# Optimization experiments

Hardware: AMD Instinct MI355X
Metric: run time of the kernel (lower is better)

## Reference

```python
import jax, jax.numpy as jnp
import numpy as np

B, LI, LJ, D = 32, 512, 512, 512
NN_DIM = 256  # agg output dim = 2*NN_DIM = 512


def setup_inputs() -> dict:
    key = jax.random.key(0)
    k1, k2, k3 = jax.random.split(key, 3)
    i = jax.random.normal(k1, (B, LI, D), dtype=jnp.float32)
    j = jax.random.normal(k2, (B, LJ, D), dtype=jnp.float32)
    W_agg = jax.random.normal(k3, (D, 2 * NN_DIM), dtype=jnp.float32) * (1.0 / np.sqrt(D))
    b_agg = jnp.zeros((2 * NN_DIM,), dtype=jnp.float32)
    return {"i": i, "j": j, "W_agg": W_agg, "b_agg": b_agg}


def _agg(x, W, b):
    # shared aggregation net: Dense(2*nn_dim) + tanh, then mean-pool over time
    # x: [B, L, D] -> [B, 2*nn_dim]
    return jnp.mean(jnp.tanh(jnp.einsum('bld,dh->blh', x, W) + b), axis=1)


def reference(i, j, W_agg, b_agg):
    # cross-attention scores: [B, Li, Lj]
    weight = jnp.einsum('bik,bjk->bij', i, j)
    # row softmax (over Lj) -> weights to aggregate j per i-position
    weight_j = jax.nn.softmax(weight, axis=2)
    # column softmax (over Li) -> weights to aggregate i per j-position
    weight_i = jax.nn.softmax(weight, axis=1)
    weighted_i = jnp.einsum('bij,bid->bjd', weight_i, i)  # [B, Lj, D]
    weighted_j = jnp.einsum('bij,bjd->bid', weight_j, j)  # [B, Li, D]
    output_i = jnp.abs(i - weighted_j)  # [B, Li, D]
    output_j = jnp.abs(j - weighted_i)  # [B, Lj, D]
    oi = _agg(output_i, W_agg, b_agg)   # [B, 2*nn_dim]
    oj = _agg(output_j, W_agg, b_agg)   # [B, 2*nn_dim]
    # K.mean(K.stack([oi, oj], axis=1), axis=1)
    return 0.5 * (oi + oj)
```

## Files before the change

kernel.cpp:

```cpp
#include <hip/hip_runtime.h>
#include <math.h>

#define B_ 32
#define L_ 512
#define D_ 512
#define H_ 512

typedef unsigned short u16;
typedef _Float16 h16;
typedef h16 half8 __attribute__((ext_vector_type(8)));
typedef float f32x4 __attribute__((ext_vector_type(4)));

#define SW(r, c) ((c) ^ (((r) >> 1) & 3))

typedef __attribute__((address_space(1))) void gvoid;
typedef __attribute__((address_space(3))) void svoid;
__device__ __forceinline__ void async_cp16(const void* g, void* l) {
    __builtin_amdgcn_global_load_lds((gvoid*)g, (svoid*)l, 16, 0, 0);
}

__device__ __forceinline__ u16 f2h(float x) {
    h16 h = (h16)x;
    u16 r;
    __builtin_memcpy(&r, &h, 2);
    return r;
}
__device__ __forceinline__ float h2f(u16 u) {
    h16 h;
    __builtin_memcpy(&h, &u, 2);
    return (float)h;
}
__device__ __forceinline__ float fast_tanh(float x) {
    return 1.0f - 2.0f / (__expf(2.0f * x) + 1.0f);
}

__device__ __forceinline__ void xcd_decode16(int n, int& z, int& tile) {
    int xcd = n & 7, w = n >> 3;
    z = xcd + 8 * (w >> 4);
    tile = w & 15;
}

__global__ __launch_bounds__(256) void cvt_all(const float* __restrict__ I,
                                               const float* __restrict__ Jm,
                                               const float* __restrict__ W,
                                               u16* __restrict__ Ih, u16* __restrict__ IhT,
                                               u16* __restrict__ Jh, u16* __restrict__ JhT,
                                               u16* __restrict__ WT,
                                               float* __restrict__ out) {
    const int z = blockIdx.z;
    const float* src;
    u16* h;
    u16* hT;
    size_t base;
    if (z < 32) {
        src = I; h = Ih; hT = IhT; base = (size_t)z * 512 * 512;
    } else if (z < 64) {
        src = Jm; h = Jh; hT = JhT; base = (size_t)(z - 32) * 512 * 512;
    } else {
        src = W; h = nullptr; hT = WT; base = 0;
        out[(blockIdx.y * 8 + blockIdx.x) * 256 + threadIdx.x] = 0.0f;
    }
    const int r0 = blockIdx.y * 64, c0 = blockIdx.x * 64;
    __shared__ u16 t[64][66];
    const int tid = threadIdx.x;
    const int tr = tid >> 4, tc4 = (tid & 15) * 4;
#pragma unroll
    for (int rep = 0; rep < 4; ++rep) {
        int r = rep * 16 + tr;
        f32x4 v = *(const f32x4*)(src + base + (size_t)(r0 + r) * 512 + c0 + tc4);
        unsigned h0 = f2h(v[0]), h1 = f2h(v[1]), h2 = f2h(v[2]), h3 = f2h(v[3]);
        if (h)
            *(uint2*)(h + base + (size_t)(r0 + r) * 512 + c0 + tc4) =
                make_uint2(h0 | (h1 << 16), h2 | (h3 << 16));
        t[r][tc4] = (u16)h0; t[r][tc4 + 1] = (u16)h1;
        t[r][tc4 + 2] = (u16)h2; t[r][tc4 + 3] = (u16)h3;
    }
    __syncthreads();
#pragma unroll
    for (int rep = 0; rep < 4; ++rep) {
        int r = rep * 16 + tr;
        unsigned a = t[tc4][r], b = t[tc4 + 1][r], c = t[tc4 + 2][r], d = t[tc4 + 3][r];
        *(uint2*)(hT + base + (size_t)(c0 + r) * 512 + r0 + tc4) =
            make_uint2(a | (b << 16), c | (d << 16));
    }
}

__global__ __launch_bounds__(256, 2) void score_mfma(const u16* __restrict__ Ih,
                                                     const u16* __restrict__ Jh,
                                                     u16* __restrict__ P_un,
                                                     u16* __restrict__ P_unT,
                                                     float* __restrict__ rtmax,
                                                     float* __restrict__ rtsum,
                                                     float* __restrict__ ctmax,
                                                     float* __restrict__ ctsum) {
    int b, tile;
    xcd_decode16(blockIdx.x, b, tile);
    const int i0 = (tile >> 2) * 128, j0 = (tile & 3) * 128;
    __shared__ u16 Ah[128 * 32], Bh[128 * 32];
    const int tid = threadIdx.x;
    const int wave = tid >> 6, lane = tid & 63;
    const int wm = (wave >> 1) * 64, wn = (wave & 1) * 64;
    const int lr = lane & 15, q = lane >> 4;
    const size_t boff = (size_t)b * L_ * D_;
    const u16* Ibh = Ih + boff;
    const u16* Jbh = Jh + boff;

    f32x4 acc[4][4] = {};

    for (int k0 = 0; k0 < D_; k0 += 32) {
#pragma unroll
        for (int h = 0; h < 2; ++h) {
            int g = wave * 2 + h;
            int r = g * 16 + (lane >> 2);
            int cg = SW(r, lane & 3);
            async_cp16(Ibh + (size_t)(i0 + r) * D_ + k0 + cg * 8, (char*)Ah + g * 1024);
            async_cp16(Jbh + (size_t)(j0 + r) * D_ + k0 + cg * 8, (char*)Bh + g * 1024);
        }
        __syncthreads();
        half8 af[4], bf[4];
#pragma unroll
        for (int mi = 0; mi < 4; ++mi) {
            int r = wm + mi * 16 + lr;
            af[mi] = *(const half8*)&Ah[r * 32 + SW(r, q) * 8];
        }
#pragma unroll
        for (int ni = 0; ni < 4; ++ni) {
            int r = wn + ni * 16 + lr;
            bf[ni] = *(const half8*)&Bh[r * 32 + SW(r, q) * 8];
        }
#pragma unroll
        for (int mi = 0; mi < 4; ++mi)
#pragma unroll
            for (int ni = 0; ni < 4; ++ni)
                acc[mi][ni] = __builtin_amdgcn_mfma_f32_16x16x32_f16(af[mi], bf[ni], acc[mi][ni], 0, 0, 0);
        __syncthreads();
    }

    float rm[4][4];
#pragma unroll
    for (int mi = 0; mi < 4; ++mi)
#pragma unroll
        for (int r4 = 0; r4 < 4; ++r4) {
            float t = fmaxf(fmaxf(acc[mi][0][r4], acc[mi][1][r4]),
                            fmaxf(acc[mi][2][r4], acc[mi][3][r4]));
#pragma unroll
            for (int off = 1; off < 16; off <<= 1) t = fmaxf(t, __shfl_xor(t, off));
            rm[mi][r4] = t;
        }
    float cm[4];
#pragma unroll
    for (int ni = 0; ni < 4; ++ni) {
        float u = -1e30f;
#pragma unroll
        for (int mi = 0; mi < 4; ++mi)
#pragma unroll
            for (int r4 = 0; r4 < 4; ++r4) u = fmaxf(u, acc[mi][ni][r4]);
        u = fmaxf(u, __shfl_xor(u, 16));
        u = fmaxf(u, __shfl_xor(u, 32));
        cm[ni] = u;
    }

    u16* Pu_b = P_un + (size_t)b * L_ * L_;
    u16* PuT_b = P_unT + (size_t)b * L_ * L_;
    float rs[4][4] = {};
    float cs[4] = {};
#pragma unroll
    for (int mi = 0; mi < 4; ++mi)
#pragma unroll
        for (int ni = 0; ni < 4; ++ni) {
            int i_base = i0 + wm + mi * 16 + q * 4;
            int j = j0 + wn + ni * 16 + lr;
            unsigned pc[4];
#pragma unroll
            for (int r4 = 0; r4 < 4; ++r4) {
                float er = __expf(acc[mi][ni][r4] - rm[mi][r4]);
                rs[mi][r4] += er;
                Pu_b[(size_t)(i_base + r4) * L_ + j] = f2h(er);
                float ec = __expf(acc[mi][ni][r4] - cm[ni]);
                cs[ni] += ec;
                pc[r4] = f2h(ec);
            }
            *(uint2*)&PuT_b[(size_t)j * L_ + i_base] =
                make_uint2(pc[0] | (pc[1] << 16), pc[2] | (pc[3] << 16));
        }

    const int gr = (j0 + wn) >> 6;
    const int gc = (i0 + wm) >> 6;
#pragma unroll
    for (int mi = 0; mi < 4; ++mi)
#pragma unroll
        for (int r4 = 0; r4 < 4; ++r4) {
            float s = rs[mi][r4];
#pragma unroll
            for (int off = 1; off < 16; off <<= 1) s += __shfl_xor(s, off);
            if (lr == 0) {
                int i = i0 + wm + mi * 16 + q * 4 + r4;
                rtmax[((size_t)b * L_ + i) * 8 + gr] = rm[mi][r4];
                rtsum[((size_t)b * L_ + i) * 8 + gr] = s;
            }
        }
#pragma unroll
    for (int ni = 0; ni < 4; ++ni) {
        float s = cs[ni];
        s += __shfl_xor(s, 16);
        s += __shfl_xor(s, 32);
        if (q == 0) {
            int j = j0 + wn + ni * 16 + lr;
            ctmax[((size_t)b * L_ + j) * 8 + gc] = cm[ni];
            ctsum[((size_t)b * L_ + j) * 8 + gc] = s;
        }
    }
}

__global__ __launch_bounds__(256, 2) void absdiff_scaled(const u16* __restrict__ P_un,
                                                         const u16* __restrict__ P_unT,
                                                         const float* __restrict__ rtmax,
                                                         const float* __restrict__ rtsum,
                                                         const float* __restrict__ ctmax,
                                                         const float* __restrict__ ctsum,
                                                         const u16* __restrict__ JhT,
                                                         const u16* __restrict__ IhT,
                                                         const u16* __restrict__ Ih,
                                                         const u16* __restrict__ Jh,
                                                         u16* __restrict__ Xall) {
    int zz, tile;
    xcd_decode16(blockIdx.x, zz, tile);
    const int side = zz >> 5, b = zz & 31;
    const int a0 = (tile >> 2) * 128, d0 = (tile & 3) * 128;
    const u16* Pb = (side ? P_unT : P_un) + (size_t)b * L_ * L_;
    const float* tmax = (side ? ctmax : rtmax) + (size_t)b * L_ * 8;
    const float* tsum = (side ? ctsum : rtsum) + (size_t)b * L_ * 8;
    const u16* Vt = (side ? IhT : JhT) + (size_t)b * D_ * L_;
    const u16* Oh = (side ? Jh : Ih) + (size_t)b * L_ * D_;
    u16* Xb = Xall + (size_t)zz * L_ * D_;

    __shared__ u16 As[128 * 32], Bs[128 * 32];
    __shared__ float sc[8][128];
    const int tid = threadIdx.x;
    const int wave = tid >> 6, lane = tid & 63;
    const int wm = (wave >> 1) * 64, wn = (wave & 1) * 64;
    const int lr = lane & 15, q = lane >> 4;

    if (tid < 128) {
        const float* tm = tmax + (size_t)(a0 + tid) * 8;
        const float* ts = tsum + (size_t)(a0 + tid) * 8;
        f32x4 m0 = *(const f32x4*)tm, m1 = *(const f32x4*)(tm + 4);
        f32x4 s0 = *(const f32x4*)ts, s1 = *(const f32x4*)(ts + 4);
        float m = fmaxf(fmaxf(fmaxf(m0[0], m0[1]), fmaxf(m0[2], m0[3])),
                        fmaxf(fmaxf(m1[0], m1[1]), fmaxf(m1[2], m1[3])));
        float e0 = __expf(m0[0] - m), e1 = __expf(m0[1] - m);
        float e2 = __expf(m0[2] - m), e3 = __expf(m0[3] - m);
        float e4 = __expf(m1[0] - m), e5 = __expf(m1[1] - m);
        float e6 = __expf(m1[2] - m), e7 = __expf(m1[3] - m);
        float inv = 1.0f / (e0 * s0[0] + e1 * s0[1] + e2 * s0[2] + e3 * s0[3] +
                            e4 * s1[0] + e5 * s1[1] + e6 * s1[2] + e7 * s1[3]);
        sc[0][tid] = e0 * inv; sc[1][tid] = e1 * inv;
        sc[2][tid] = e2 * inv; sc[3][tid] = e3 * inv;
        sc[4][tid] = e4 * inv; sc[5][tid] = e5 * inv;
        sc[6][tid] = e6 * inv; sc[7][tid] = e7 * inv;
    }
    __syncthreads();

    f32x4 acc[4][4] = {};

    for (int k0 = 0; k0 < L_; k0 += 32) {
#pragma unroll
        for (int h = 0; h < 2; ++h) {
            int g = wave * 2 + h;
            int r = g * 16 + (lane >> 2);
            int cg = SW(r, lane & 3);
            async_cp16(Pb + (size_t)(a0 + r) * L_ + k0 + cg * 8, (char*)As + g * 1024);
            async_cp16(Vt + (size_t)(d0 + r) * L_ + k0 + cg * 8, (char*)Bs + g * 1024);
        }
        __syncthreads();
        const int gk = k0 >> 6;
        half8 af[4], bf[4];
#pragma unroll
        for (int mi = 0; mi < 4; ++mi) {
            int r = wm + mi * 16 + lr;
            h16 s = (h16)sc[gk][r];
            half8 s8 = {s, s, s, s, s, s, s, s};
            af[mi] = *(const half8*)&As[r * 32 + SW(r, q) * 8] * s8;
        }
#pragma unroll
        for (int ni = 0; ni < 4; ++ni) {
            int r = wn + ni * 16 + lr;
            bf[ni] = *(const half8*)&Bs[r * 32 + SW(r, q) * 8];
        }
#pragma unroll
        for (int mi = 0; mi < 4; ++mi)
#pragma unroll
            for (int ni = 0; ni < 4; ++ni)
                acc[mi][ni] = __builtin_amdgcn_mfma_f32_16x16x32_f16(af[mi], bf[ni], acc[mi][ni], 0, 0, 0);
        __syncthreads();
    }

#pragma unroll
    for (int mi = 0; mi < 4; ++mi)
#pragma unroll
        for (int ni = 0; ni < 4; ++ni) {
            int i = a0 + wm + mi * 16 + q * 4;
            int d = d0 + wn + ni * 16 + lr;
#pragma unroll
            for (int r4 = 0; r4 < 4; ++r4) {
                float x = fabsf(h2f(Oh[(size_t)(i + r4) * D_ + d]) - acc[mi][ni][r4]);
                Xb[(size_t)(i + r4) * D_ + d] = f2h(x);
            }
        }
}

__global__ __launch_bounds__(256, 2) void agg_mfma(const u16* __restrict__ Xall,
                                                   const u16* __restrict__ Wt,
                                                   const float* __restrict__ bias,
                                                   float* __restrict__ out) {
    int zz, tile;
    xcd_decode16(blockIdx.x, zz, tile);
    const int bb = zz & 31;
    const u16* Xb = Xall + (size_t)zz * L_ * D_;
    const int l0 = (tile >> 2) * 128, h0 = (tile & 3) * 128;
    __shared__ u16 As[128 * 32], Bs[128 * 32];
    const int tid = threadIdx.x;
    const int wave = tid >> 6, lane = tid & 63;
    const int wm = (wave >> 1) * 64, wn = (wave & 1) * 64;
    const int lr = lane & 15, q = lane >> 4;

    f32x4 acc[4][4] = {};

    for (int k0 = 0; k0 < D_; k0 += 32) {
#pragma unroll
        for (int h = 0; h < 2; ++h) {
            int g = wave * 2 + h;
            int r = g * 16 + (lane >> 2);
            int cg = SW(r, lane & 3);
            async_cp16(Xb + (size_t)(l0 + r) * D_ + k0 + cg * 8, (char*)As + g * 1024);
            async_cp16(Wt + (size_t)(h0 + r) * D_ + k0 + cg * 8, (char*)Bs + g * 1024);
        }
        __syncthreads();
        half8 af[4], bf[4];
#pragma unroll
        for (int mi = 0; mi < 4; ++mi) {
            int r = wm + mi * 16 + lr;
            af[mi] = *(const half8*)&As[r * 32 + SW(r, q) * 8];
        }
#pragma unroll
        for (int ni = 0; ni < 4; ++ni) {
            int r = wn + ni * 16 + lr;
            bf[ni] = *(const half8*)&Bs[r * 32 + SW(r, q) * 8];
        }
#pragma unroll
        for (int mi = 0; mi < 4; ++mi)
#pragma unroll
            for (int ni = 0; ni < 4; ++ni)
                acc[mi][ni] = __builtin_amdgcn_mfma_f32_16x16x32_f16(af[mi], bf[ni], acc[mi][ni], 0, 0, 0);
        __syncthreads();
    }

#pragma unroll
    for (int ni = 0; ni < 4; ++ni) {
        int hcol = h0 + wn + ni * 16 + lr;
        float bsv = bias[hcol];
        float ssum = 0.f;
#pragma unroll
        for (int mi = 0; mi < 4; ++mi)
#pragma unroll
            for (int r4 = 0; r4 < 4; ++r4)
                ssum += fast_tanh(acc[mi][ni][r4] + bsv);
        ssum += __shfl_xor(ssum, 16);
        ssum += __shfl_xor(ssum, 32);
        if (q == 0) atomicAdd(&out[bb * H_ + hcol], ssum * (0.5f / (float)L_));
    }
}

extern "C" void kernel_launch(void* const* d_in, const int* in_sizes, int n_in,
                              void* d_out, int out_size, void* d_ws, size_t ws_size,
                              hipStream_t stream) {
    const float* I = (const float*)d_in[0];
    const float* Jm = (const float*)d_in[1];
    const float* W = (const float*)d_in[2];
    const float* bias = (const float*)d_in[3];
    float* out = (float*)d_out;

    const size_t BLD = (size_t)B_ * L_ * D_;
    const size_t BLL = (size_t)B_ * L_ * L_;

    char* p = (char*)d_ws;
    auto give = [&](size_t bytes) {
        char* r = p;
        p += (bytes + 255) & ~(size_t)255;
        return r;
    };
    u16* Ih = (u16*)give(BLD * 2);
    u16* Jh = (u16*)give(BLD * 2);
    u16* IhT = (u16*)give(BLD * 2);
    u16* JhT = (u16*)give(BLD * 2);
    u16* WT = (u16*)give((size_t)D_ * H_ * 2);
    u16* P_un = (u16*)give(BLL * 2);
    u16* P_unT = (u16*)give(BLL * 2);
    float* rtmax = (float*)give((size_t)B_ * L_ * 8 * 4);
    float* rtsum = (float*)give((size_t)B_ * L_ * 8 * 4);
    float* ctmax = (float*)give((size_t)B_ * L_ * 8 * 4);
    float* ctsum = (float*)give((size_t)B_ * L_ * 8 * 4);
    u16* Xall = (u16*)give(2 * BLD * 2);

    cvt_all<<<dim3(8, 8, 65), 256, 0, stream>>>(I, Jm, W, Ih, IhT, Jh, JhT, WT, out);
    score_mfma<<<512, 256, 0, stream>>>(Ih, Jh, P_un, P_unT, rtmax, rtsum, ctmax, ctsum);
    absdiff_scaled<<<1024, 256, 0, stream>>>(P_un, P_unT, rtmax, rtsum, ctmax, ctsum,
                                             JhT, IhT, Ih, Jh, Xall);
    agg_mfma<<<1024, 256, 0, stream>>>(Xall, WT, bias, out);
}
```

Measured before the change: 197.5 us.

## Fuse absdiff GEMM and aggregation GEMM into one kernel via LDS-resident X tile

```diff
diff --git a/kernel.cpp b/kernel.cpp
--- a/kernel.cpp
+++ b/kernel.cpp
@@ -212,38 +212,40 @@
     }
 }
 
-__global__ __launch_bounds__(256, 2) void absdiff_scaled(const u16* __restrict__ P_un,
-                                                         const u16* __restrict__ P_unT,
-                                                         const float* __restrict__ rtmax,
-                                                         const float* __restrict__ rtsum,
-                                                         const float* __restrict__ ctmax,
-                                                         const float* __restrict__ ctsum,
-                                                         const u16* __restrict__ JhT,
-                                                         const u16* __restrict__ IhT,
-                                                         const u16* __restrict__ Ih,
-                                                         const u16* __restrict__ Jh,
-                                                         u16* __restrict__ Xall) {
-    int zz, tile;
-    xcd_decode16(blockIdx.x, zz, tile);
+__global__ __launch_bounds__(512, 2) void absagg(
+    const u16* __restrict__ P_un, const u16* __restrict__ P_unT,
+    const float* __restrict__ rtmax, const float* __restrict__ rtsum,
+    const float* __restrict__ ctmax, const float* __restrict__ ctsum,
+    const u16* __restrict__ JhT, const u16* __restrict__ IhT,
+    const u16* __restrict__ Ih, const u16* __restrict__ Jh,
+    const u16* __restrict__ Wt, const float* __restrict__ bias,
+    float* __restrict__ out) {
+    const int n = blockIdx.x;
+    const int xcd = n & 7, w = n >> 3;
+    const int zz = xcd + 8 * (w >> 3);
+    const int tile = w & 7;
     const int side = zz >> 5, b = zz & 31;
-    const int a0 = (tile >> 2) * 128, d0 = (tile & 3) * 128;
+    const int l0 = tile * 64;
+
     const u16* Pb = (side ? P_unT : P_un) + (size_t)b * L_ * L_;
     const float* tmax = (side ? ctmax : rtmax) + (size_t)b * L_ * 8;
     const float* tsum = (side ? ctsum : rtsum) + (size_t)b * L_ * 8;
-    const u16* Vt = (side ? IhT : JhT) + (size_t)b * D_ * L_;
+    const u16* Vt = (side ? IhT : JhT) + (size_t)b * (size_t)D_ * L_;
     const u16* Oh = (side ? Jh : Ih) + (size_t)b * L_ * D_;
-    u16* Xb = Xall + (size_t)zz * L_ * D_;
-
-    __shared__ u16 As[128 * 32], Bs[128 * 32];
-    __shared__ float sc[8][128];
+
+    __shared__ u16 stage[2][18432];
+    __shared__ u16 Xs[64 * 512];
+    __shared__ float sc[8][64];
+
     const int tid = threadIdx.x;
     const int wave = tid >> 6, lane = tid & 63;
-    const int wm = (wave >> 1) * 64, wn = (wave & 1) * 64;
     const int lr = lane & 15, q = lane >> 4;
-
-    if (tid < 128) {
-        const float* tm = tmax + (size_t)(a0 + tid) * 8;
-        const float* ts = tsum + (size_t)(a0 + tid) * 8;
+    const int wl = (wave >> 2) * 32;
+    const int wc = (wave & 3) * 128;
+
+    if (tid < 64) {
+        const float* tm = tmax + (size_t)(l0 + tid) * 8;
+        const float* ts = tsum + (size_t)(l0 + tid) * 8;
         f32x4 m0 = *(const f32x4*)tm, m1 = *(const f32x4*)(tm + 4);
         f32x4 s0 = *(const f32x4*)ts, s1 = *(const f32x4*)(ts + 4);
         float m = fmaxf(fmaxf(fmaxf(m0[0], m0[1]), fmaxf(m0[2], m0[3])),
@@ -259,115 +261,121 @@
         sc[4][tid] = e4 * inv; sc[5][tid] = e5 * inv;
         sc[6][tid] = e6 * inv; sc[7][tid] = e7 * inv;
     }
+
+    auto stageA = [&](int t, int bufi) {
+        const int k0 = t * 32;
+        char* buf = (char*)&stage[bufi][0];
+        if (wave < 4) {
+            int r = wave * 16 + (lane >> 2);
+            int cg = SW(r, lane & 3);
+            async_cp16(Pb + (size_t)(l0 + r) * L_ + k0 + cg * 8, buf + 32768 + wave * 1024);
+        }
+#pragma unroll
+        for (int i = 0; i < 4; ++i) {
+            int c = wave * 4 + i;
+            int dR = c * 16 + (lane >> 2);
+            int cg = SW(dR, lane & 3);
+            async_cp16(Vt + (size_t)dR * L_ + k0 + cg * 8, buf + c * 1024);
+        }
+    };
+    auto stageB = [&](int t, int bufi) {
+        const int k0 = t * 32;
+        char* buf = (char*)&stage[bufi][0];
+#pragma unroll
+        for (int i = 0; i < 4; ++i) {
+            int c = wave * 4 + i;
+            int hR = c * 16 + (lane >> 2);
+            int cg = SW(hR, lane & 3);
+            async_cp16(Wt + (size_t)hR * D_ + k0 + cg * 8, buf + c * 1024);
+        }
+    };
+
+    f32x4 acc[2][8] = {};
+
+    stageA(0, 0);
     __syncthreads();
-
-    f32x4 acc[4][4] = {};
-
-    for (int k0 = 0; k0 < L_; k0 += 32) {
-#pragma unroll
-        for (int h = 0; h < 2; ++h) {
-            int g = wave * 2 + h;
-            int r = g * 16 + (lane >> 2);
-            int cg = SW(r, lane & 3);
-            async_cp16(Pb + (size_t)(a0 + r) * L_ + k0 + cg * 8, (char*)As + g * 1024);
-            async_cp16(Vt + (size_t)(d0 + r) * L_ + k0 + cg * 8, (char*)Bs + g * 1024);
-        }
-        __syncthreads();
-        const int gk = k0 >> 6;
-        half8 af[4], bf[4];
-#pragma unroll
-        for (int mi = 0; mi < 4; ++mi) {
-            int r = wm + mi * 16 + lr;
+#pragma unroll 2
+    for (int t = 0; t < 16; ++t) {
+        if (t < 15) stageA(t + 1, (t + 1) & 1);
+        const u16* buf = &stage[t & 1][0];
+        const int gk = t >> 1;
+        half8 af[2], bf[8];
+#pragma unroll
+        for (int mi = 0; mi < 2; ++mi) {
+            int r = wl + mi * 16 + lr;
             h16 s = (h16)sc[gk][r];
             half8 s8 = {s, s, s, s, s, s, s, s};
-            af[mi] = *(const half8*)&As[r * 32 + SW(r, q) * 8] * s8;
-        }
-#pragma unroll
-        for (int ni = 0; ni < 4; ++ni) {
-            int r = wn + ni * 16 + lr;
-            bf[ni] = *(const half8*)&Bs[r * 32 + SW(r, q) * 8];
-        }
-#pragma unroll
-        for (int mi = 0; mi < 4; ++mi)
-#pragma unroll
-            for (int ni = 0; ni < 4; ++ni)
+            af[mi] = *(const half8*)&buf[16384 + r * 32 + SW(r, q) * 8] * s8;
+        }
+#pragma unroll
+        for (int ni = 0; ni < 8; ++ni) {
+            int dR = wc + ni * 16 + lr;
+            bf[ni] = *(const half8*)&buf[dR * 32 + SW(dR, q) * 8];
+        }
+#pragma unroll
+        for (int mi = 0; mi < 2; ++mi)
+#pragma unroll
+            for (int ni = 0; ni < 8; ++ni)
                 acc[mi][ni] = __builtin_amdgcn_mfma_f32_16x16x32_f16(af[mi], bf[ni], acc[mi][ni], 0, 0, 0);
-        __syncthreads();
-    }
-
-#pragma unroll
-    for (int mi = 0; mi < 4; ++mi)
-#pragma unroll
-        for (int ni = 0; ni < 4; ++ni) {
-            int i = a0 + wm + mi * 16 + q * 4;
-            int d = d0 + wn + ni * 16 + lr;
+        if (t < 15) __syncthreads();
+    }
+
+    const f32x4 vzero = {0.f, 0.f, 0.f, 0.f};
+#pragma unroll
+    for (int mi = 0; mi < 2; ++mi)
+#pragma unroll
+        for (int ni = 0; ni < 8; ++ni) {
+            const int ll = wl + mi * 16 + q * 4;
+            const int d = wc + ni * 16 + lr;
 #pragma unroll
             for (int r4 = 0; r4 < 4; ++r4) {
-                float x = fabsf(h2f(Oh[(size_t)(i + r4) * D_ + d]) - acc[mi][ni][r4]);
-                Xb[(size_t)(i + r4) * D_ + d] = f2h(x);
+                const int l = ll + r4;
+                float x = fabsf(h2f(Oh[(size_t)(l0 + l) * D_ + d]) - acc[mi][ni][r4]);
+                *(u16*)((char*)Xs + (((l * 512 + d) * 2) ^ ((l & 7) << 4))) = f2h(x);
             }
-        }
-}
-
-__global__ __launch_bounds__(256, 2) void agg_mfma(const u16* __restrict__ Xall,
-                                                   const u16* __restrict__ Wt,
-                                                   const float* __restrict__ bias,
-                                                   float* __restrict__ out) {
-    int zz, tile;
-    xcd_decode16(blockIdx.x, zz, tile);
-    const int bb = zz & 31;
-    const u16* Xb = Xall + (size_t)zz * L_ * D_;
-    const int l0 = (tile >> 2) * 128, h0 = (tile & 3) * 128;
-    __shared__ u16 As[128 * 32], Bs[128 * 32];
-    const int tid = threadIdx.x;
-    const int wave = tid >> 6, lane = tid & 63;
-    const int wm = (wave >> 1) * 64, wn = (wave & 1) * 64;
-    const int lr = lane & 15, q = lane >> 4;
-
-    f32x4 acc[4][4] = {};
-
-    for (int k0 = 0; k0 < D_; k0 += 32) {
-#pragma unroll
-        for (int h = 0; h < 2; ++h) {
-            int g = wave * 2 + h;
-            int r = g * 16 + (lane >> 2);
-            int cg = SW(r, lane & 3);
-            async_cp16(Xb + (size_t)(l0 + r) * D_ + k0 + cg * 8, (char*)As + g * 1024);
-            async_cp16(Wt + (size_t)(h0 + r) * D_ + k0 + cg * 8, (char*)Bs + g * 1024);
-        }
-        __syncthreads();
-        half8 af[4], bf[4];
-#pragma unroll
-        for (int mi = 0; mi < 4; ++mi) {
-            int r = wm + mi * 16 + lr;
-            af[mi] = *(const half8*)&As[r * 32 + SW(r, q) * 8];
-        }
-#pragma unroll
-        for (int ni = 0; ni < 4; ++ni) {
-            int r = wn + ni * 16 + lr;
-            bf[ni] = *(const half8*)&Bs[r * 32 + SW(r, q) * 8];
-        }
-#pragma unroll
-        for (int mi = 0; mi < 4; ++mi)
-#pragma unroll
-            for (int ni = 0; ni < 4; ++ni)
+            acc[mi][ni] = vzero;
+        }
+
+    stageB(0, 0);
+    __syncthreads();
+
+#pragma unroll 2
+    for (int t = 0; t < 16; ++t) {
+        if (t < 15) stageB(t + 1, (t + 1) & 1);
+        const u16* buf = &stage[t & 1][0];
+        const int k0 = t * 32;
+        half8 af[2], bf[8];
+#pragma unroll
+        for (int mi = 0; mi < 2; ++mi) {
+            int l = wl + mi * 16 + lr;
+            af[mi] = *(const half8*)((const char*)Xs + ((l * 1024 + k0 * 2 + q * 16) ^ ((l & 7) << 4)));
+        }
+#pragma unroll
+        for (int ni = 0; ni < 8; ++ni) {
+            int hR = wc + ni * 16 + lr;
+            bf[ni] = *(const half8*)&buf[hR * 32 + SW(hR, q) * 8];
+        }
+#pragma unroll
+        for (int mi = 0; mi < 2; ++mi)
+#pragma unroll
+            for (int ni = 0; ni < 8; ++ni)
                 acc[mi][ni] = __builtin_amdgcn_mfma_f32_16x16x32_f16(af[mi], bf[ni], acc[mi][ni], 0, 0, 0);
-        __syncthreads();
-    }
-
-#pragma unroll
-    for (int ni = 0; ni < 4; ++ni) {
-        int hcol = h0 + wn + ni * 16 + lr;
-        float bsv = bias[hcol];
+        if (t < 15) __syncthreads();
+    }
+
+#pragma unroll
+    for (int ni = 0; ni < 8; ++ni) {
+        const int hcol = wc + ni * 16 + lr;
+        const float bsv = bias[hcol];
         float ssum = 0.f;
 #pragma unroll
-        for (int mi = 0; mi < 4; ++mi)
+        for (int mi = 0; mi < 2; ++mi)
 #pragma unroll
             for (int r4 = 0; r4 < 4; ++r4)
                 ssum += fast_tanh(acc[mi][ni][r4] + bsv);
         ssum += __shfl_xor(ssum, 16);
         ssum += __shfl_xor(ssum, 32);
-        if (q == 0) atomicAdd(&out[bb * H_ + hcol], ssum * (0.5f / (float)L_));
+        if (q == 0) atomicAdd(&out[b * H_ + hcol], ssum * (0.5f / (float)L_));
     }
 }
 
@@ -400,11 +408,9 @@
     float* rtsum = (float*)give((size_t)B_ * L_ * 8 * 4);
     float* ctmax = (float*)give((size_t)B_ * L_ * 8 * 4);
     float* ctsum = (float*)give((size_t)B_ * L_ * 8 * 4);
-    u16* Xall = (u16*)give(2 * BLD * 2);
 
     cvt_all<<<dim3(8, 8, 65), 256, 0, stream>>>(I, Jm, W, Ih, IhT, Jh, JhT, WT, out);
     score_mfma<<<512, 256, 0, stream>>>(Ih, Jh, P_un, P_unT, rtmax, rtsum, ctmax, ctsum);
-    absdiff_scaled<<<1024, 256, 0, stream>>>(P_un, P_unT, rtmax, rtsum, ctmax, ctsum,
-                                             JhT, IhT, Ih, Jh, Xall);
-    agg_mfma<<<1024, 256, 0, stream>>>(Xall, WT, bias, out);
-}
+    absagg<<<512, 512, 0, stream>>>(P_un, P_unT, rtmax, rtsum, ctmax, ctsum,
+                                    JhT, IhT, Ih, Jh, WT, bias, out);
+}
```

Result: slower. 206.3 us (+4.5%).

## Rewrite aggregation GEMM as 256x256-tile, 8-phase double-buffered pipelined kernel

Applied to the files above, without the earlier changes.

```diff
diff --git a/kernel.cpp b/kernel.cpp
--- a/kernel.cpp
+++ b/kernel.cpp
@@ -309,66 +309,121 @@
         }
 }
 
-__global__ __launch_bounds__(256, 2) void agg_mfma(const u16* __restrict__ Xall,
-                                                   const u16* __restrict__ Wt,
-                                                   const float* __restrict__ bias,
-                                                   float* __restrict__ out) {
-    int zz, tile;
-    xcd_decode16(blockIdx.x, zz, tile);
+__global__ __launch_bounds__(512, 2) void agg_8ph(const u16* __restrict__ Xall,
+                                                  const u16* __restrict__ Wt,
+                                                  const float* __restrict__ bias,
+                                                  float* __restrict__ out) {
+    const int bid = blockIdx.x;
+    const int n = bid >> 3;
+    const int zz = (bid & 7) + 8 * (n >> 2);
+    const int tile = n & 3;
     const int bb = zz & 31;
-    const u16* Xb = Xall + (size_t)zz * L_ * D_;
-    const int l0 = (tile >> 2) * 128, h0 = (tile & 3) * 128;
-    __shared__ u16 As[128 * 32], Bs[128 * 32];
+    const int l0 = (tile >> 1) * 256, h0 = (tile & 1) * 256;
+    const u16* Xb = Xall + (size_t)zz * L_ * D_ + (size_t)l0 * D_;
+    const u16* Wb = Wt + (size_t)h0 * D_;
+
+    __shared__ u16 AL[2][2][8192];
+    __shared__ u16 BL[2][2][8192];
+
     const int tid = threadIdx.x;
     const int wave = tid >> 6, lane = tid & 63;
-    const int wm = (wave >> 1) * 64, wn = (wave & 1) * 64;
     const int lr = lane & 15, q = lane >> 4;
-
-    f32x4 acc[4][4] = {};
-
-    for (int k0 = 0; k0 < D_; k0 += 32) {
-#pragma unroll
-        for (int h = 0; h < 2; ++h) {
-            int g = wave * 2 + h;
-            int r = g * 16 + (lane >> 2);
-            int cg = SW(r, lane & 3);
-            async_cp16(Xb + (size_t)(l0 + r) * D_ + k0 + cg * 8, (char*)As + g * 1024);
-            async_cp16(Wt + (size_t)(h0 + r) * D_ + k0 + cg * 8, (char*)Bs + g * 1024);
-        }
-        __syncthreads();
-        half8 af[4], bf[4];
-#pragma unroll
-        for (int mi = 0; mi < 4; ++mi) {
-            int r = wm + mi * 16 + lr;
-            af[mi] = *(const half8*)&As[r * 32 + SW(r, q) * 8];
-        }
-#pragma unroll
-        for (int ni = 0; ni < 4; ++ni) {
-            int r = wn + ni * 16 + lr;
-            bf[ni] = *(const half8*)&Bs[r * 32 + SW(r, q) * 8];
-        }
-#pragma unroll
-        for (int mi = 0; mi < 4; ++mi)
-#pragma unroll
-            for (int ni = 0; ni < 4; ++ni)
-                acc[mi][ni] = __builtin_amdgcn_mfma_f32_16x16x32_f16(af[mi], bf[ni], acc[mi][ni], 0, 0, 0);
-        __syncthreads();
+    const int wr = wave >> 2, wc4 = wave & 3;
+
+    const int ch0 = wave * 2;
+    const int phys = lane * 16;
+    const int Lb = phys ^ (((phys >> 6) & 3) << 4);
+    const int sr = Lb >> 6;
+    const int sk = (Lb & 63) >> 1;
+
+#define ST_A(t, kh)                                                                     \
+    do {                                                                                \
+        char* dst_ = (char*)&AL[(t) & 1][(kh)][0];                                      \
+        const u16* s_ = Xb + (t) * 64 + (kh) * 32 + sk;                                 \
+        async_cp16(s_ + (size_t)(ch0 * 16 + sr) * D_, dst_ + ch0 * 1024);               \
+        async_cp16(s_ + (size_t)(ch0 * 16 + 16 + sr) * D_, dst_ + ch0 * 1024 + 1024);   \
+    } while (0)
+#define ST_B(t, kh)                                                                     \
+    do {                                                                                \
+        char* dst_ = (char*)&BL[(t) & 1][(kh)][0];                                      \
+        const u16* s_ = Wb + (t) * 64 + (kh) * 32 + sk;                                 \
+        async_cp16(s_ + (size_t)(ch0 * 16 + sr) * D_, dst_ + ch0 * 1024);               \
+        async_cp16(s_ + (size_t)(ch0 * 16 + 16 + sr) * D_, dst_ + ch0 * 1024 + 1024);   \
+    } while (0)
+
+    f32x4 acc[8][4] = {};
+
+#define PHASE(t, mh, kk, STAGE_STMT, WAIT_STMT)                                         \
+    do {                                                                                \
+        const char* Ah_ = (const char*)&AL[(t) & 1][(kk)][0];                           \
+        const char* Bh_ = (const char*)&BL[(t) & 1][(kk)][0];                           \
+        half8 a_[4], b_[4];                                                             \
+        _Pragma("unroll") for (int mi = 0; mi < 4; ++mi) {                              \
+            int r_ = wr * 128 + (mh)*64 + mi * 16 + lr;                                 \
+            a_[mi] = *(const half8*)(Ah_ + r_ * 64 + ((q * 16) ^ ((r_ & 3) << 4)));     \
+        }                                                                               \
+        _Pragma("unroll") for (int ni = 0; ni < 4; ++ni) {                              \
+            int r_ = wc4 * 64 + ni * 16 + lr;                                           \
+            b_[ni] = *(const half8*)(Bh_ + r_ * 64 + ((q * 16) ^ ((r_ & 3) << 4)));     \
+        }                                                                               \
+        STAGE_STMT;                                                                     \
+        asm volatile("" ::: "memory");                                                  \
+        __builtin_amdgcn_s_barrier();                                                   \
+        asm volatile("" ::: "memory");                                                  \
+        __builtin_amdgcn_s_setprio(1);                                                  \
+        _Pragma("unroll") for (int mi = 0; mi < 4; ++mi)                                \
+            _Pragma("unroll") for (int ni = 0; ni < 4; ++ni)                            \
+                acc[(mh)*4 + mi][ni] = __builtin_amdgcn_mfma_f32_16x16x32_f16(          \
+                    a_[mi], b_[ni], acc[(mh)*4 + mi][ni], 0, 0, 0);                     \
+        __builtin_amdgcn_s_setprio(0);                                                  \
+        WAIT_STMT;                                                                      \
+        asm volatile("" ::: "memory");                                                  \
+        __builtin_amdgcn_s_barrier();                                                   \
+        asm volatile("" ::: "memory");                                                  \
+    } while (0)
+
+#define VM4 asm volatile("s_waitcnt vmcnt(4)" ::: "memory")
+#define VM0 asm volatile("s_waitcnt vmcnt(0)" ::: "memory")
+
+    ST_A(0, 0); ST_B(0, 0); ST_A(0, 1); ST_B(0, 1);
+    ST_A(1, 0); ST_B(1, 0);
+    VM4;
+    asm volatile("" ::: "memory");
+    __builtin_amdgcn_s_barrier();
+    asm volatile("" ::: "memory");
+
+    for (int it = 0; it < 4; ++it) {
+        const int T = 2 * it, U = T + 1;
+        const bool lastit = (it == 3);
+        PHASE(T, 0, 0, { ST_A(U, 1); }, {});
+        PHASE(T, 1, 0, { ST_B(U, 1); }, {});
+        PHASE(T, 0, 1, { if (!lastit) ST_A(T + 2, 0); }, {});
+        PHASE(T, 1, 1, { if (!lastit) ST_B(T + 2, 0); }, { if (lastit) VM0; else VM4; });
+        PHASE(U, 0, 0, { if (!lastit) ST_A(T + 2, 1); }, {});
+        PHASE(U, 1, 0, { if (!lastit) ST_B(T + 2, 1); }, {});
+        PHASE(U, 0, 1, { if (!lastit) ST_A(T + 3, 0); }, {});
+        PHASE(U, 1, 1, { if (!lastit) ST_B(T + 3, 0); }, { if (!lastit) VM4; });
     }
 
 #pragma unroll
     for (int ni = 0; ni < 4; ++ni) {
-        int hcol = h0 + wn + ni * 16 + lr;
-        float bsv = bias[hcol];
+        const int h = h0 + wc4 * 64 + ni * 16 + lr;
+        const float bsv = bias[h];
         float ssum = 0.f;
 #pragma unroll
-        for (int mi = 0; mi < 4; ++mi)
+        for (int mI = 0; mI < 8; ++mI)
 #pragma unroll
             for (int r4 = 0; r4 < 4; ++r4)
-                ssum += fast_tanh(acc[mi][ni][r4] + bsv);
+                ssum += fast_tanh(acc[mI][ni][r4] + bsv);
         ssum += __shfl_xor(ssum, 16);
         ssum += __shfl_xor(ssum, 32);
-        if (q == 0) atomicAdd(&out[bb * H_ + hcol], ssum * (0.5f / (float)L_));
-    }
+        if (q == 0) atomicAdd(&out[bb * H_ + h], ssum * (0.5f / (float)L_));
+    }
+#undef PHASE
+#undef ST_A
+#undef ST_B
+#undef VM4
+#undef VM0
 }
 
 extern "C" void kernel_launch(void* const* d_in, const int* in_sizes, int n_in,
@@ -406,5 +461,5 @@
     score_mfma<<<512, 256, 0, stream>>>(Ih, Jh, P_un, P_unT, rtmax, rtsum, ctmax, ctsum);
     absdiff_scaled<<<1024, 256, 0, stream>>>(P_un, P_unT, rtmax, rtsum, ctmax, ctsum,
                                              JhT, IhT, Ih, Jh, Xall);
-    agg_mfma<<<1024, 256, 0, stream>>>(Xall, WT, bias, out);
-}
+    agg_8ph<<<256, 512, 0, stream>>>(Xall, WT, bias, out);
+}
```

Result: no change. 195.7 us (-0.9%).

## Triple-buffer LDS tiles with async prefetch in absdiff and agg GEMMs

Applied to the files above, without the earlier changes.

```diff
diff --git a/kernel.cpp b/kernel.cpp
--- a/kernel.cpp
+++ b/kernel.cpp
@@ -212,30 +212,28 @@
     }
 }
 
-__global__ __launch_bounds__(256, 2) void absdiff_scaled(const u16* __restrict__ P_un,
-                                                         const u16* __restrict__ P_unT,
-                                                         const float* __restrict__ rtmax,
-                                                         const float* __restrict__ rtsum,
-                                                         const float* __restrict__ ctmax,
-                                                         const float* __restrict__ ctsum,
-                                                         const u16* __restrict__ JhT,
-                                                         const u16* __restrict__ IhT,
-                                                         const u16* __restrict__ Ih,
-                                                         const u16* __restrict__ Jh,
-                                                         u16* __restrict__ Xall) {
+__global__ __launch_bounds__(256, 3) void absdiff_t3(
+    const u16* __restrict__ P_un, const u16* __restrict__ P_unT,
+    const float* __restrict__ rtmax, const float* __restrict__ rtsum,
+    const float* __restrict__ ctmax, const float* __restrict__ ctsum,
+    const u16* __restrict__ JhT, const u16* __restrict__ IhT,
+    const u16* __restrict__ Ih, const u16* __restrict__ Jh,
+    u16* __restrict__ Xall) {
     int zz, tile;
     xcd_decode16(blockIdx.x, zz, tile);
     const int side = zz >> 5, b = zz & 31;
     const int a0 = (tile >> 2) * 128, d0 = (tile & 3) * 128;
-    const u16* Pb = (side ? P_unT : P_un) + (size_t)b * L_ * L_;
+    const u16* Pb = (side ? P_unT : P_un) + (size_t)b * L_ * L_ + (size_t)a0 * L_;
     const float* tmax = (side ? ctmax : rtmax) + (size_t)b * L_ * 8;
     const float* tsum = (side ? ctsum : rtsum) + (size_t)b * L_ * 8;
-    const u16* Vt = (side ? IhT : JhT) + (size_t)b * D_ * L_;
+    const u16* Vtb = (side ? IhT : JhT) + (size_t)b * (size_t)D_ * L_ + (size_t)d0 * L_;
     const u16* Oh = (side ? Jh : Ih) + (size_t)b * L_ * D_;
     u16* Xb = Xall + (size_t)zz * L_ * D_;
 
-    __shared__ u16 As[128 * 32], Bs[128 * 32];
-    __shared__ float sc[8][128];
+    __shared__ u16 AL[3][128 * 32];
+    __shared__ u16 BL[3][128 * 32];
+    __shared__ h16 sclh[8][128];
+
     const int tid = threadIdx.x;
     const int wave = tid >> 6, lane = tid & 63;
     const int wm = (wave >> 1) * 64, wn = (wave & 1) * 64;
@@ -254,46 +252,72 @@
         float e6 = __expf(m1[2] - m), e7 = __expf(m1[3] - m);
         float inv = 1.0f / (e0 * s0[0] + e1 * s0[1] + e2 * s0[2] + e3 * s0[3] +
                             e4 * s1[0] + e5 * s1[1] + e6 * s1[2] + e7 * s1[3]);
-        sc[0][tid] = e0 * inv; sc[1][tid] = e1 * inv;
-        sc[2][tid] = e2 * inv; sc[3][tid] = e3 * inv;
-        sc[4][tid] = e4 * inv; sc[5][tid] = e5 * inv;
-        sc[6][tid] = e6 * inv; sc[7][tid] = e7 * inv;
-    }
-    __syncthreads();
+        sclh[0][tid] = (h16)(e0 * inv); sclh[1][tid] = (h16)(e1 * inv);
+        sclh[2][tid] = (h16)(e2 * inv); sclh[3][tid] = (h16)(e3 * inv);
+        sclh[4][tid] = (h16)(e4 * inv); sclh[5][tid] = (h16)(e5 * inv);
+        sclh[6][tid] = (h16)(e6 * inv); sclh[7][tid] = (h16)(e7 * inv);
+    }
+
+    const int ch0 = wave * 2;
+    const int phys = lane * 16;
+    const int Lb = phys ^ (((phys >> 6) & 3) << 4);
+    const int sr = Lb >> 6;
+    const int sk = (Lb & 63) >> 1;
+
+#define ST2(t, SRC, DSTARR)                                                             \
+    do {                                                                                \
+        char* dst_ = (char*)&DSTARR[(t) % 3][0];                                        \
+        const u16* s_ = (SRC) + (t) * 32 + sk;                                          \
+        async_cp16(s_ + (size_t)(ch0 * 16 + sr) * 512, dst_ + ch0 * 1024);              \
+        async_cp16(s_ + (size_t)(ch0 * 16 + 16 + sr) * 512, dst_ + ch0 * 1024 + 1024);  \
+    } while (0)
 
     f32x4 acc[4][4] = {};
 
-    for (int k0 = 0; k0 < L_; k0 += 32) {
-#pragma unroll
-        for (int h = 0; h < 2; ++h) {
-            int g = wave * 2 + h;
-            int r = g * 16 + (lane >> 2);
-            int cg = SW(r, lane & 3);
-            async_cp16(Pb + (size_t)(a0 + r) * L_ + k0 + cg * 8, (char*)As + g * 1024);
-            async_cp16(Vt + (size_t)(d0 + r) * L_ + k0 + cg * 8, (char*)Bs + g * 1024);
-        }
-        __syncthreads();
-        const int gk = k0 >> 6;
+    ST2(0, Pb, AL); ST2(0, Vtb, BL);
+    ST2(1, Pb, AL); ST2(1, Vtb, BL);
+    asm volatile("s_waitcnt lgkmcnt(0)" ::: "memory");
+    asm volatile("s_waitcnt vmcnt(4)" ::: "memory");
+    asm volatile("" ::: "memory");
+    __builtin_amdgcn_s_barrier();
+    asm volatile("" ::: "memory");
+
+#pragma unroll
+    for (int t = 0; t < 16; ++t) {
+        const char* Ab = (const char*)&AL[t % 3][0];
+        const char* Bb = (const char*)&BL[t % 3][0];
         half8 af[4], bf[4];
 #pragma unroll
         for (int mi = 0; mi < 4; ++mi) {
-            int r = wm + mi * 16 + lr;
-            h16 s = (h16)sc[gk][r];
+            int r_ = wm + mi * 16 + lr;
+            half8 av = *(const half8*)(Ab + r_ * 64 + ((q * 16) ^ ((r_ & 3) << 4)));
+            h16 s = sclh[t >> 1][r_];
             half8 s8 = {s, s, s, s, s, s, s, s};
-            af[mi] = *(const half8*)&As[r * 32 + SW(r, q) * 8] * s8;
+            af[mi] = av * s8;
         }
 #pragma unroll
         for (int ni = 0; ni < 4; ++ni) {
-            int r = wn + ni * 16 + lr;
-            bf[ni] = *(const half8*)&Bs[r * 32 + SW(r, q) * 8];
-        }
+            int r_ = wn + ni * 16 + lr;
+            bf[ni] = *(const half8*)(Bb + r_ * 64 + ((q * 16) ^ ((r_ & 3) << 4)));
+        }
+        if (t + 2 < 16) { ST2(t + 2, Pb, AL); ST2(t + 2, Vtb, BL); }
+        asm volatile("" ::: "memory");
+        __builtin_amdgcn_s_barrier();
+        asm volatile("" ::: "memory");
+        __builtin_amdgcn_s_setprio(1);
 #pragma unroll
         for (int mi = 0; mi < 4; ++mi)
 #pragma unroll
             for (int ni = 0; ni < 4; ++ni)
                 acc[mi][ni] = __builtin_amdgcn_mfma_f32_16x16x32_f16(af[mi], bf[ni], acc[mi][ni], 0, 0, 0);
-        __syncthreads();
-    }
+        __builtin_amdgcn_s_setprio(0);
+        if (t < 14) asm volatile("s_waitcnt vmcnt(4)" ::: "memory");
+        else if (t == 14) asm volatile("s_waitcnt vmcnt(0)" ::: "memory");
+        asm volatile("" ::: "memory");
+        __builtin_amdgcn_s_barrier();
+        asm volatile("" ::: "memory");
+    }
+#undef ST2
 
 #pragma unroll
     for (int mi = 0; mi < 4; ++mi)
@@ -309,51 +333,81 @@
         }
 }
 
-__global__ __launch_bounds__(256, 2) void agg_mfma(const u16* __restrict__ Xall,
-                                                   const u16* __restrict__ Wt,
-                                                   const float* __restrict__ bias,
-                                                   float* __restrict__ out) {
+__global__ __launch_bounds__(256, 3) void agg_t3(const u16* __restrict__ Xall,
+                                                 const u16* __restrict__ Wt,
+                                                 const float* __restrict__ bias,
+                                                 float* __restrict__ out) {
     int zz, tile;
     xcd_decode16(blockIdx.x, zz, tile);
     const int bb = zz & 31;
-    const u16* Xb = Xall + (size_t)zz * L_ * D_;
     const int l0 = (tile >> 2) * 128, h0 = (tile & 3) * 128;
-    __shared__ u16 As[128 * 32], Bs[128 * 32];
+    const u16* Xb = Xall + (size_t)zz * L_ * D_ + (size_t)l0 * D_;
+    const u16* Wb = Wt + (size_t)h0 * D_;
+
+    __shared__ u16 AL[3][128 * 32];
+    __shared__ u16 BL[3][128 * 32];
+
     const int tid = threadIdx.x;
     const int wave = tid >> 6, lane = tid & 63;
     const int wm = (wave >> 1) * 64, wn = (wave & 1) * 64;
     const int lr = lane & 15, q = lane >> 4;
 
+    const int ch0 = wave * 2;
+    const int phys = lane * 16;
+    const int Lb = phys ^ (((phys >> 6) & 3) << 4);
+    const int sr = Lb >> 6;
+    const int sk = (Lb & 63) >> 1;
+
+#define ST2(t, SRC, DSTARR)                                                             \
+    do {                                                                                \
+        char* dst_ = (char*)&DSTARR[(t) % 3][0];                                        \
+        const u16* s_ = (SRC) + (t) * 32 + sk;                                          \
+        async_cp16(s_ + (size_t)(ch0 * 16 + sr) * 512, dst_ + ch0 * 1024);              \
+        async_cp16(s_ + (size_t)(ch0 * 16 + 16 + sr) * 512, dst_ + ch0 * 1024 + 1024);  \
+    } while (0)
+
     f32x4 acc[4][4] = {};
 
-    for (int k0 = 0; k0 < D_; k0 += 32) {
-#pragma unroll
-        for (int h = 0; h < 2; ++h) {
-            int g = wave * 2 + h;
-            int r = g * 16 + (lane >> 2);
-            int cg = SW(r, lane & 3);
-            async_cp16(Xb + (size_t)(l0 + r) * D_ + k0 + cg * 8, (char*)As + g * 1024);
-            async_cp16(Wt + (size_t)(h0 + r) * D_ + k0 + cg * 8, (char*)Bs + g * 1024);
-        }
-        __syncthreads();
+    ST2(0, Xb, AL); ST2(0, Wb, BL);
+    ST2(1, Xb, AL); ST2(1, Wb, BL);
+    asm volatile("s_waitcnt vmcnt(4)" ::: "memory");
+    asm volatile("" ::: "memory");
+    __builtin_amdgcn_s_barrier();
+    asm volatile("" ::: "memory");
+
+#pragma unroll
+    for (int t = 0; t < 16; ++t) {
+        const char* Ab = (const char*)&AL[t % 3][0];
+        const char* Bb = (const char*)&BL[t % 3][0];
         half8 af[4], bf[4];
 #pragma unroll
         for (int mi = 0; mi < 4; ++mi) {
-            int r = wm + mi * 16 + lr;
-            af[mi] = *(const half8*)&As[r * 32 + SW(r, q) * 8];
+            int r_ = wm + mi * 16 + lr;
+            af[mi] = *(const half8*)(Ab + r_ * 64 + ((q * 16) ^ ((r_ & 3) << 4)));
         }
 #pragma unroll
         for (int ni = 0; ni < 4; ++ni) {
-            int r = wn + ni * 16 + lr;
-            bf[ni] = *(const half8*)&Bs[r * 32 + SW(r, q) * 8];
-        }
+            int r_ = wn + ni * 16 + lr;
+            bf[ni] = *(const half8*)(Bb + r_ * 64 + ((q * 16) ^ ((r_ & 3) << 4)));
+        }
+        if (t + 2 < 16) { ST2(t + 2, Xb, AL); ST2(t + 2, Wb, BL); }
+        asm volatile("" ::: "memory");
+        __builtin_amdgcn_s_barrier();
+        asm volatile("" ::: "memory");
+        __builtin_amdgcn_s_setprio(1);
 #pragma unroll
         for (int mi = 0; mi < 4; ++mi)
 #pragma unroll
             for (int ni = 0; ni < 4; ++ni)
                 acc[mi][ni] = __builtin_amdgcn_mfma_f32_16x16x32_f16(af[mi], bf[ni], acc[mi][ni], 0, 0, 0);
-        __syncthreads();
-    }
+        __builtin_amdgcn_s_setprio(0);
+        if (t < 14) asm volatile("s_waitcnt vmcnt(4)" ::: "memory");
+        else if (t == 14) asm volatile("s_waitcnt vmcnt(0)" ::: "memory");
+        asm volatile("" ::: "memory");
+        __builtin_amdgcn_s_barrier();
+        asm volatile("" ::: "memory");
+    }
+#undef ST2
 
 #pragma unroll
     for (int ni = 0; ni < 4; ++ni) {
@@ -404,7 +458,7 @@
 
     cvt_all<<<dim3(8, 8, 65), 256, 0, stream>>>(I, Jm, W, Ih, IhT, Jh, JhT, WT, out);
     score_mfma<<<512, 256, 0, stream>>>(Ih, Jh, P_un, P_unT, rtmax, rtsum, ctmax, ctsum);
-    absdiff_scaled<<<1024, 256, 0, stream>>>(P_un, P_unT, rtmax, rtsum, ctmax, ctsum,
-                                             JhT, IhT, Ih, Jh, Xall);
-    agg_mfma<<<1024, 256, 0, stream>>>(Xall, WT, bias, out);
-}
+    absdiff_t3<<<1024, 256, 0, stream>>>(P_un, P_unT, rtmax, rtsum, ctmax, ctsum,
+                                         JhT, IhT, Ih, Jh, Xall);
+    agg_t3<<<1024, 256, 0, stream>>>(Xall, WT, bias, out);
+}
```

Result: no change. 196.8 us (-0.4%).
